# Optimization experiments

Hardware: AMD Instinct MI355X
Metric: run time of the kernel (lower is better)

The kernel has to match this reference:

```python
import jax, jax.numpy as jnp
import numpy as np

B, N, L, D = 256, 128, 2048, 64
ATOM_V, AMINO_V = 2000, 10000
LAYER_GNN, LAYER_CNN, LAYER_OUT = 3, 3, 2
SIDE = 5
WINDOW = 2 * SIDE + 1   # 11 -> conv kernel 23x23, padding 11
N_OUT = 2
EPS = 1e-6


def setup_inputs() -> dict:
    ks = jax.random.split(jax.random.key(0), 16)
    s = 0.05
    return {
        "atoms": jax.random.randint(ks[0], (B, N), 0, ATOM_V),
        "atoms_mask": jnp.ones((B, N), jnp.float32),
        "adjacency": jax.random.uniform(ks[1], (B, N, N), jnp.float32),
        "amino": jax.random.randint(ks[2], (B, L), 0, AMINO_V),
        "amino_mask": jnp.ones((B, L), jnp.float32),
        "emb_fp": jax.random.normal(ks[3], (ATOM_V, D), jnp.float32) * s,
        "emb_word": jax.random.normal(ks[4], (AMINO_V, D), jnp.float32) * s,
        "W_gnn": jax.random.normal(ks[5], (LAYER_GNN, D, D), jnp.float32) * s,
        "b_gnn": jax.random.normal(ks[6], (LAYER_GNN, D), jnp.float32) * s,
        "conv_k": jax.random.normal(ks[7], (LAYER_CNN, 2 * WINDOW + 1, 2 * WINDOW + 1), jnp.float32) * s,
        "conv_b": jax.random.normal(ks[8], (LAYER_CNN,), jnp.float32) * s,
        "W_att": jax.random.normal(ks[9], (D, D), jnp.float32) * s,
        "b_att": jax.random.normal(ks[10], (D,), jnp.float32) * s,
        "W_out": jax.random.normal(ks[11], (LAYER_OUT, 2 * D, 2 * D), jnp.float32) * s,
        "b_out": jax.random.normal(ks[12], (LAYER_OUT, 2 * D), jnp.float32) * s,
        "W_int": jax.random.normal(ks[13], (N_OUT, 2 * D), jnp.float32) * s,
        "b_int": jax.random.normal(ks[14], (N_OUT,), jnp.float32) * s,
    }


def reference(atoms, atoms_mask, adjacency, amino, amino_mask,
              emb_fp, emb_word, W_gnn, b_gnn, conv_k, conv_b,
              W_att, b_att, W_out, b_out, W_int, b_int):
    # ---- compound vector via GNN over dense adjacency ----
    xs = emb_fp[atoms]                                   # [B,N,D]
    for i in range(LAYER_GNN):
        hs = jax.nn.relu(jnp.einsum('bnd,ed->bne', xs, W_gnn[i]) + b_gnn[i])
        xs = xs + jnp.einsum('bnm,bmd->bnd', adjacency, hs)
    am = atoms_mask[..., None]                           # [B,N,1]
    compound = (jnp.sum(xs * am, axis=1) / (jnp.sum(am, axis=1) + EPS))[:, None, :]  # [B,1,D]

    # ---- protein vector via attention-CNN ----
    ps = emb_word[amino][:, None]                        # [B,1,L,D] (NCHW)
    for i in range(LAYER_CNN):
        y = jax.lax.conv_general_dilated(
            ps, conv_k[i][None, None], (1, 1),
            [(WINDOW, WINDOW), (WINDOW, WINDOW)],
            dimension_numbers=('NCHW', 'OIHW', 'NCHW'))
        ps = jax.nn.relu(y + conv_b[i])
    ps = ps[:, 0]                                        # [B,L,D]
    h = jax.nn.relu(jnp.einsum('bqd,ed->bqe', compound, W_att) + b_att)  # [B,1,D]
    hs = jax.nn.relu(jnp.einsum('bld,ed->ble', ps, W_att) + b_att)       # [B,L,D]
    pm = amino_mask[..., None]                           # [B,L,1]
    hs = hs * pm
    weights = jnp.tanh(jnp.einsum('bqd,bld->bql', h, hs))  # [B,1,L]
    ys = jnp.transpose(weights, (0, 2, 1)) * hs             # [B,L,D]
    protein = (jnp.sum(ys, axis=1) / (jnp.sum(pm, axis=1) + EPS))[:, None, :]  # [B,1,D]

    # ---- fuse and predict ----
    cat = jnp.concatenate([compound, protein], axis=2)[:, 0]  # [B,2D]
    for j in range(LAYER_OUT):
        cat = jax.nn.relu(cat @ W_out[j].T + b_out[j])  # dropout is identity in eval
    return cat @ W_int.T + b_int                          # [B,N_OUT]
```

## Files before the change

### kernel.cpp

```cpp
#include <hip/hip_runtime.h>
#include <hip/hip_bf16.h>
#include <cstdint>
#include <cstddef>

#define BB 256
#define NN 128
#define LL 2048
#define DD 64
#define KS 23
#define CPAD 12
#define EPSF 1e-6f
#define ACH 8

typedef __bf16 v8bf __attribute__((ext_vector_type(8)));
typedef float v4f __attribute__((ext_vector_type(4)));

__device__ __forceinline__ float bf2f(uint32_t u) {
  union { uint32_t i; float f; } c; c.i = u << 16; return c.f;
}
__device__ __forceinline__ uint16_t f2bf(float f) {
  union { float f; uint32_t i; } c; c.f = f;
  uint32_t i = c.i;
  return (uint16_t)((i + 0x7fffu + ((i >> 16) & 1u)) >> 16);
}
__device__ __forceinline__ __bf16 f2bf16(float f) {
  union { uint16_t u; __bf16 h; } c; c.u = f2bf(f); return c.h;
}
__device__ __forceinline__ v8bf cvt8(float4 f0, float4 f1) {
  v8bf r;
  r[0] = (__bf16)f0.x; r[1] = (__bf16)f0.y; r[2] = (__bf16)f0.z; r[3] = (__bf16)f0.w;
  r[4] = (__bf16)f1.x; r[5] = (__bf16)f1.y; r[6] = (__bf16)f1.z; r[7] = (__bf16)f1.w;
  return r;
}

#define XSS 68
#define HTS3 136

__global__ __launch_bounds__(256) void gnn_kernel(
    const int* __restrict__ atoms, const float* __restrict__ atoms_mask,
    const float* __restrict__ adj, const float* __restrict__ emb_fp,
    const float* __restrict__ W_gnn, const float* __restrict__ b_gnn,
    const float* __restrict__ W_att, const float* __restrict__ b_att,
    float* __restrict__ compound, float* __restrict__ hvec_g)
{
  __shared__ float xs[NN * XSS];
  __shared__ uint16_t hsT[DD * HTS3];
  __shared__ float mask_s[NN];
  __shared__ float psum[4][64];
  __shared__ float cvec[64];

  const int b = blockIdx.x;
  const int tid = threadIdx.x;
  const int lane = tid & 63;
  const int w = tid >> 6;
  const int m16 = lane & 15;
  const int s = lane >> 4;

  for (int idx = tid; idx < NN * 16; idx += 256) {
    int n = idx >> 4, c4 = idx & 15;
    int a = atoms[b * NN + n];
    float4 v = ((const float4*)(emb_fp + (size_t)a * DD))[c4];
    *(float4*)(xs + n * XSS + c4 * 4) = v;
  }
  if (tid < NN) mask_s[tid] = atoms_mask[b * NN + tid];
  __syncthreads();

  const int row0 = 32 * w;
  for (int layer = 0; layer < 3; ++layer) {
    v8bf Wf[2][4];
    float bias[4];
    const float* Wl = W_gnn + (size_t)layer * DD * DD;
    #pragma unroll
    for (int nt = 0; nt < 4; ++nt) {
      bias[nt] = b_gnn[layer * DD + nt * 16 + m16];
      #pragma unroll
      for (int kc = 0; kc < 2; ++kc) {
        const float* p = Wl + (size_t)(nt * 16 + m16) * DD + kc * 32 + s * 8;
        Wf[kc][nt] = cvt8(((const float4*)p)[0], ((const float4*)p)[1]);
      }
    }
    float4 araw[8][2];
    const float* adjw = adj + ((size_t)b * NN + row0) * NN;
    #pragma unroll
    for (int kc = 0; kc < 4; ++kc)
      #pragma unroll
      for (int mt = 0; mt < 2; ++mt) {
        const float* p = adjw + (size_t)(mt * 16 + m16) * NN + kc * 32 + s * 8;
        araw[kc * 2 + mt][0] = ((const float4*)p)[0];
        araw[kc * 2 + mt][1] = ((const float4*)p)[1];
      }

    v4f acc[2][4];
    #pragma unroll
    for (int mt = 0; mt < 2; ++mt)
      #pragma unroll
      for (int nt = 0; nt < 4; ++nt)
        acc[mt][nt] = (v4f){bias[nt], bias[nt], bias[nt], bias[nt]};
    #pragma unroll
    for (int kc = 0; kc < 2; ++kc) {
      v8bf Axs[2];
      #pragma unroll
      for (int mt = 0; mt < 2; ++mt) {
        const float* p = xs + (size_t)(row0 + mt * 16 + m16) * XSS + kc * 32 + s * 8;
        Axs[mt] = cvt8(((const float4*)p)[0], ((const float4*)p)[1]);
      }
      #pragma unroll
      for (int mt = 0; mt < 2; ++mt)
        #pragma unroll
        for (int nt = 0; nt < 4; ++nt)
          acc[mt][nt] = __builtin_amdgcn_mfma_f32_16x16x32_bf16(
              Axs[mt], Wf[kc][nt], acc[mt][nt], 0, 0, 0);
    }
    __syncthreads();
    #pragma unroll
    for (int mt = 0; mt < 2; ++mt)
      #pragma unroll
      for (int nt = 0; nt < 4; ++nt) {
        int e = nt * 16 + m16;
        int m = row0 + mt * 16 + s * 4;
        union { uint64_t u; __bf16 h[4]; } pk;
        #pragma unroll
        for (int r = 0; r < 4; ++r)
          pk.h[r] = (__bf16)fmaxf(acc[mt][nt][r], 0.f);
        *(uint64_t*)(hsT + (size_t)e * HTS3 + m) = pk.u;
      }
    __syncthreads();

    v4f acc2[2][4];
    #pragma unroll
    for (int mt = 0; mt < 2; ++mt)
      #pragma unroll
      for (int nt = 0; nt < 4; ++nt)
        #pragma unroll
        for (int r = 0; r < 4; ++r)
          acc2[mt][nt][r] = xs[(size_t)(row0 + mt * 16 + s * 4 + r) * XSS + nt * 16 + m16];
    #pragma unroll
    for (int kc = 0; kc < 4; ++kc) {
      v8bf Aa[2];
      #pragma unroll
      for (int mt = 0; mt < 2; ++mt)
        Aa[mt] = cvt8(araw[kc * 2 + mt][0], araw[kc * 2 + mt][1]);
      v8bf Bh[4];
      #pragma unroll
      for (int nt = 0; nt < 4; ++nt)
        Bh[nt] = *(const v8bf*)(hsT + (size_t)(nt * 16 + m16) * HTS3 + kc * 32 + s * 8);
      #pragma unroll
      for (int mt = 0; mt < 2; ++mt)
        #pragma unroll
        for (int nt = 0; nt < 4; ++nt)
          acc2[mt][nt] = __builtin_amdgcn_mfma_f32_16x16x32_bf16(
              Aa[mt], Bh[nt], acc2[mt][nt], 0, 0, 0);
    }
    #pragma unroll
    for (int mt = 0; mt < 2; ++mt)
      #pragma unroll
      for (int nt = 0; nt < 4; ++nt)
        #pragma unroll
        for (int r = 0; r < 4; ++r)
          xs[(size_t)(row0 + mt * 16 + s * 4 + r) * XSS + nt * 16 + m16] = acc2[mt][nt][r];
  }

  float pr = 0.f;
  for (int i = 0; i < 32; ++i) {
    int n = row0 + i;
    pr = fmaf(mask_s[n], xs[(size_t)n * XSS + lane], pr);
  }
  psum[w][lane] = pr;
  __syncthreads();
  if (tid < 64) {
    float ssum = psum[0][tid] + psum[1][tid] + psum[2][tid] + psum[3][tid];
    float den = 0.f;
    #pragma unroll 8
    for (int i = 0; i < NN; ++i) den += mask_s[i];
    float c = ssum / (den + EPSF);
    compound[b * DD + tid] = c;
    cvec[tid] = c;
  }
  __syncthreads();
  if (tid < 64) {
    float a = b_att[tid];
    const float* wr = W_att + (size_t)tid * DD;
    #pragma unroll
    for (int d4 = 0; d4 < 16; ++d4) {
      float4 w4 = ((const float4*)wr)[d4];
      float4 c4 = ((const float4*)cvec)[d4];
      a = fmaf(w4.x, c4.x, a); a = fmaf(w4.y, c4.y, a);
      a = fmaf(w4.z, c4.z, a); a = fmaf(w4.w, c4.w, a);
    }
    hvec_g[b * DD + tid] = fmaxf(a, 0.f);
  }
}

__global__ __launch_bounds__(64) void bfrag_kernel(
    const float* __restrict__ conv_k, uint16_t* __restrict__ btab)
{
  const int layer = blockIdx.x;
  const int lane = threadIdx.x;
  const int s = lane >> 4, n = lane & 15;
  for (int kk = 0; kk < 30; ++kk) {
    int k8 = kk * 4 + s;
    int i = k8 / 5;
    int c8 = k8 - i * 5;
    #pragma unroll
    for (int j = 0; j < 8; ++j) {
      int c = c8 * 8 + j;
      int jj = c - n - 1;
      float v = (i < KS && jj >= 0 && jj < KS)
                    ? conv_k[layer * KS * KS + i * KS + jj] : 0.f;
      btab[(((size_t)layer * 30 + kk) * 64 + lane) * 8 + j] = f2bf(v);
    }
  }
}

#define TW 88
#define TROWS 86

__global__ __launch_bounds__(256, 2) void conv_mfma_kernel(
    const uint16_t* __restrict__ in, uint16_t* __restrict__ out,
    const uint16_t* __restrict__ btab, const float* __restrict__ conv_b,
    const int* __restrict__ amino, const float* __restrict__ emb_word,
    int layer, int gmode)
{
  __shared__ uint16_t tile[TROWS * TW];
  const int tid = threadIdx.x;
  const int l0 = blockIdx.x * 64;
  const int b  = blockIdx.y;
  const int lane = tid & 63;
  const int g = tid >> 6;

  v8bf bfr[30];
  const uint16_t* bt = btab + (size_t)layer * 30 * 512 + lane * 8;
  #pragma unroll
  for (int kk = 0; kk < 30; ++kk)
    bfr[kk] = *(const v8bf*)(bt + kk * 512);

  for (int i = tid; i < TROWS * 6; i += 256) {
    int r = i / 6, h = i - r * 6;
    int off = (h < 3) ? h * 4 : 76 + (h - 3) * 4;
    *(uint2*)(tile + r * TW + off) = make_uint2(0u, 0u);
  }
  const uint16_t* inb = in + (size_t)b * LL * DD;
  for (int idx = tid; idx < TROWS * 8; idx += 256) {
    int t = idx >> 3, c8 = idx & 7;
    int gl = l0 - 11 + t;
    uint16_t* dst = tile + t * TW + CPAD + c8 * 8;
    if (gl >= 0 && gl < LL) {
      if (gmode) {
        int a = amino[b * LL + gl];
        const float* src = emb_word + (size_t)a * DD + c8 * 8;
        float4 f0 = ((const float4*)src)[0];
        float4 f1 = ((const float4*)src)[1];
        union { uint2 u2[2]; uint16_t h[8]; } pk;
        pk.h[0] = f2bf(f0.x); pk.h[1] = f2bf(f0.y);
        pk.h[2] = f2bf(f0.z); pk.h[3] = f2bf(f0.w);
        pk.h[4] = f2bf(f1.x); pk.h[5] = f2bf(f1.y);
        pk.h[6] = f2bf(f1.z); pk.h[7] = f2bf(f1.w);
        *(uint2*)(dst)     = pk.u2[0];
        *(uint2*)(dst + 4) = pk.u2[1];
      } else {
        uint4 v = *(const uint4*)(inb + (size_t)gl * DD + c8 * 8);
        *(uint2*)(dst)     = make_uint2(v.x, v.y);
        *(uint2*)(dst + 4) = make_uint2(v.z, v.w);
      }
    } else {
      *(uint2*)(dst)     = make_uint2(0u, 0u);
      *(uint2*)(dst + 4) = make_uint2(0u, 0u);
    }
  }
  __syncthreads();

  const int s = lane >> 4;
  const int m16 = lane & 15;
  v4f acc[4];
  #pragma unroll
  for (int m = 0; m < 4; ++m) acc[m] = (v4f){0.f, 0.f, 0.f, 0.f};

  #pragma unroll
  for (int kk = 0; kk < 30; ++kk) {
    int k8 = kk * 4 + s;
    int i = k8 / 5;
    int c8 = k8 - i * 5;
    const uint16_t* ap = tile + (m16 + i) * TW + 16 * g + c8 * 8;
    v8bf a0 = *(const v8bf*)(ap);
    v8bf a1 = *(const v8bf*)(ap + 16 * TW);
    v8bf a2 = *(const v8bf*)(ap + 32 * TW);
    v8bf a3 = *(const v8bf*)(ap + 48 * TW);
    acc[0] = __builtin_amdgcn_mfma_f32_16x16x32_bf16(a0, bfr[kk], acc[0], 0, 0, 0);
    acc[1] = __builtin_amdgcn_mfma_f32_16x16x32_bf16(a1, bfr[kk], acc[1], 0, 0, 0);
    acc[2] = __builtin_amdgcn_mfma_f32_16x16x32_bf16(a2, bfr[kk], acc[2], 0, 0, 0);
    acc[3] = __builtin_amdgcn_mfma_f32_16x16x32_bf16(a3, bfr[kk], acc[3], 0, 0, 0);
  }

  const float bias = conv_b[layer];
  uint16_t* outb = out + ((size_t)b * LL + l0) * DD + 16 * g + m16;
  #pragma unroll
  for (int m = 0; m < 4; ++m) {
    #pragma unroll
    for (int r = 0; r < 4; ++r) {
      int row = m * 16 + s * 4 + r;
      outb[(size_t)row * DD] = f2bf(fmaxf(acc[m][r] + bias, 0.f));
    }
  }
}

#define HTS2 66

__global__ __launch_bounds__(256) void attn_part_kernel(
    const uint16_t* __restrict__ ps, const float* __restrict__ amino_mask,
    const float* __restrict__ hvec_g, const float* __restrict__ W_att,
    const float* __restrict__ b_att, float* __restrict__ pacc_part,
    float* __restrict__ msum_part)
{
  __shared__ float ht[4][32 * HTS2];
  __shared__ float pm_s[4][64];
  __shared__ float wv_s[4][32];
  __shared__ float hv_s[64];

  const int chunk = blockIdx.x;
  const int b = blockIdx.y;
  const int tid = threadIdx.x;
  const int lane = tid & 63;
  const int w = tid >> 6;
  const int m16 = lane & 15;
  const int s = lane >> 4;

  v8bf bfrB[2][4];
  float bias[4];
  #pragma unroll
  for (int nt = 0; nt < 4; ++nt) {
    bias[nt] = b_att[nt * 16 + m16];
    const float* wr = W_att + (size_t)(nt * 16 + m16) * DD + s * 8;
    #pragma unroll
    for (int kc = 0; kc < 2; ++kc) {
      float4 f0 = ((const float4*)(wr + kc * 32))[0];
      float4 f1 = ((const float4*)(wr + kc * 32))[1];
      bfrB[kc][nt] = cvt8(f0, f1);
    }
  }
  if (tid < 64) hv_s[tid] = hvec_g[b * DD + tid];

  const int rowbase = chunk * 256 + w * 64;
  const float* pmb = amino_mask + (size_t)b * LL;
  pm_s[w][lane] = pmb[rowbase + lane];
  const float macc = pm_s[w][lane];
  __syncthreads();

  float pacc[4] = {0.f, 0.f, 0.f, 0.f};
  const uint16_t* psb = ps + ((size_t)b * LL + rowbase) * DD;

  #pragma unroll
  for (int step = 0; step < 2; ++step) {
    const uint16_t* pr = psb + (size_t)step * 32 * DD;
    v8bf A[2][2];
    #pragma unroll
    for (int mt = 0; mt < 2; ++mt)
      #pragma unroll
      for (int kc = 0; kc < 2; ++kc)
        A[mt][kc] = *(const v8bf*)(pr + (mt * 16 + m16) * DD + kc * 32 + s * 8);

    v4f acc[2][4];
    #pragma unroll
    for (int mt = 0; mt < 2; ++mt)
      #pragma unroll
      for (int nt = 0; nt < 4; ++nt)
        acc[mt][nt] = (v4f){0.f, 0.f, 0.f, 0.f};
    #pragma unroll
    for (int kc = 0; kc < 2; ++kc)
      #pragma unroll
      for (int mt = 0; mt < 2; ++mt)
        #pragma unroll
        for (int nt = 0; nt < 4; ++nt)
          acc[mt][nt] = __builtin_amdgcn_mfma_f32_16x16x32_bf16(
              A[mt][kc], bfrB[kc][nt], acc[mt][nt], 0, 0, 0);

    float vals[2][4][4];
    float* htw = ht[w];
    #pragma unroll
    for (int mt = 0; mt < 2; ++mt)
      #pragma unroll
      for (int r = 0; r < 4; ++r) {
        int row = mt * 16 + s * 4 + r;
        float pm = pm_s[w][step * 32 + row];
        #pragma unroll
        for (int nt = 0; nt < 4; ++nt) {
          float v = fmaxf(acc[mt][nt][r] + bias[nt], 0.f) * pm;
          vals[mt][nt][r] = v;
          htw[row * HTS2 + nt * 16 + m16] = v;
        }
      }
    __syncthreads();

    {
      int row = lane & 31, eh = lane >> 5;
      const float* hr = ht[w] + row * HTS2 + eh * 32;
      const float* hv = hv_s + eh * 32;
      float d = 0.f;
      #pragma unroll
      for (int t = 0; t < 8; ++t) {
        float4 hh = *(const float4*)(hr + 4 * t);
        float4 vv = *(const float4*)(hv + 4 * t);
        d = fmaf(hh.x, vv.x, d); d = fmaf(hh.y, vv.y, d);
        d = fmaf(hh.z, vv.z, d); d = fmaf(hh.w, vv.w, d);
      }
      d += __shfl_xor(d, 32);
      float wt = tanhf(d);
      if (lane < 32) wv_s[w][row] = wt;
    }
    __syncthreads();

    #pragma unroll
    for (int mt = 0; mt < 2; ++mt)
      #pragma unroll
      for (int r = 0; r < 4; ++r) {
        float wt = wv_s[w][mt * 16 + s * 4 + r];
        #pragma unroll
        for (int nt = 0; nt < 4; ++nt)
          pacc[nt] = fmaf(wt, vals[mt][nt][r], pacc[nt]);
      }
    __syncthreads();
  }

  const size_t idx = ((size_t)b * ACH + chunk) * 4 + w;
  #pragma unroll
  for (int nt = 0; nt < 4; ++nt) {
    float p = pacc[nt];
    p += __shfl_xor(p, 16);
    p += __shfl_xor(p, 32);
    if (m16 == lane)
      pacc_part[idx * 64 + nt * 16 + lane] = p;
  }
  float m = macc;
  #pragma unroll
  for (int off = 1; off < 64; off <<= 1) m += __shfl_xor(m, off);
  if (lane == 0) msum_part[idx] = m;
}

__global__ __launch_bounds__(128) void attn_final_kernel(
    const float* __restrict__ compound, const float* __restrict__ pacc_part,
    const float* __restrict__ msum_part, const float* __restrict__ W_out,
    const float* __restrict__ b_out, const float* __restrict__ W_int,
    const float* __restrict__ b_int, float* __restrict__ outp)
{
  __shared__ float cat[128];
  __shared__ float cat2[128];
  const int b = blockIdx.x;
  const int tid = threadIdx.x;

  if (tid < 64) {
    float p = 0.f, den = 0.f;
    #pragma unroll 4
    for (int c = 0; c < ACH * 4; ++c) {
      p += pacc_part[((size_t)b * ACH * 4 + c) * 64 + tid];
      den += msum_part[b * ACH * 4 + c];
    }
    cat[tid] = compound[b * DD + tid];
    cat[64 + tid] = p / (den + EPSF);
  }
  __syncthreads();
  {
    float a = b_out[tid];
    const float* wr = W_out + (size_t)tid * 128;
    #pragma unroll 8
    for (int dd = 0; dd < 128; ++dd) a = fmaf(wr[dd], cat[dd], a);
    cat2[tid] = fmaxf(a, 0.f);
  }
  __syncthreads();
  {
    float a = b_out[128 + tid];
    const float* wr = W_out + 128 * 128 + (size_t)tid * 128;
    #pragma unroll 8
    for (int dd = 0; dd < 128; ++dd) a = fmaf(wr[dd], cat2[dd], a);
    __syncthreads();
    cat[tid] = fmaxf(a, 0.f);
  }
  __syncthreads();
  if (tid < 2) {
    float a = b_int[tid];
    const float* wr = W_int + (size_t)tid * 128;
    #pragma unroll 8
    for (int dd = 0; dd < 128; ++dd) a = fmaf(wr[dd], cat[dd], a);
    outp[b * 2 + tid] = a;
  }
}

extern "C" void kernel_launch(void* const* d_in, const int* in_sizes, int n_in,
                              void* d_out, int out_size, void* d_ws, size_t ws_size,
                              hipStream_t stream) {
  const int*   atoms      = (const int*)d_in[0];
  const float* atoms_mask = (const float*)d_in[1];
  const float* adjacency  = (const float*)d_in[2];
  const int*   amino      = (const int*)d_in[3];
  const float* amino_mask = (const float*)d_in[4];
  const float* emb_fp     = (const float*)d_in[5];
  const float* emb_word   = (const float*)d_in[6];
  const float* W_gnn      = (const float*)d_in[7];
  const float* b_gnn      = (const float*)d_in[8];
  const float* conv_k     = (const float*)d_in[9];
  const float* conv_b     = (const float*)d_in[10];
  const float* W_att      = (const float*)d_in[11];
  const float* b_att      = (const float*)d_in[12];
  const float* W_out      = (const float*)d_in[13];
  const float* b_out      = (const float*)d_in[14];
  const float* W_int      = (const float*)d_in[15];
  const float* b_int      = (const float*)d_in[16];
  float* out = (float*)d_out;

  char* ws = (char*)d_ws;
  const size_t ps_bytes = (size_t)BB * LL * DD * 2;
  float*    compound  = (float*)ws;
  uint16_t* ps_a      = (uint16_t*)(ws + 65536);
  uint16_t* ps_b      = (uint16_t*)(ws + 65536 + ps_bytes);
  uint16_t* btab      = (uint16_t*)(ws + 65536 + 2 * ps_bytes);
  float*    hvec_g    = (float*)(ws + 65536 + 2 * ps_bytes + 131072);
  float*    pacc_part = (float*)ps_a;
  float*    msum_part = (float*)((char*)ps_a + (size_t)BB * ACH * 4 * 64 * 4);

  bfrag_kernel<<<3, 64, 0, stream>>>(conv_k, btab);
  gnn_kernel<<<BB, 256, 0, stream>>>(atoms, atoms_mask, adjacency, emb_fp,
                                     W_gnn, b_gnn, W_att, b_att,
                                     compound, hvec_g);
  conv_mfma_kernel<<<dim3(LL / 64, BB), 256, 0, stream>>>(ps_a, ps_b, btab, conv_b,
                                                          amino, emb_word, 0, 1);
  conv_mfma_kernel<<<dim3(LL / 64, BB), 256, 0, stream>>>(ps_b, ps_a, btab, conv_b,
                                                          amino, emb_word, 1, 0);
  conv_mfma_kernel<<<dim3(LL / 64, BB), 256, 0, stream>>>(ps_a, ps_b, btab, conv_b,
                                                          amino, emb_word, 2, 0);
  attn_part_kernel<<<dim3(ACH, BB), 256, 0, stream>>>(ps_b, amino_mask, hvec_g,
                                                      W_att, b_att,
                                                      pacc_part, msum_part);
  attn_final_kernel<<<BB, 128, 0, stream>>>(compound, pacc_part, msum_part,
                                            W_out, b_out, W_int, b_int, out);
}
```

Before: 421.8 us.

## Fuse GNN into first conv launch and fuse last conv with attention

The GNN work now runs as an extra column of blocks inside the first conv launch, so it overlaps with the convolution instead of running as its own kernel. The third conv layer is fused with the attention-partial computation: the conv output tile is written to shared memory as bf16 and fed straight into the W_att MFMA, tanh weighting and partial sums. This removes a full write and re-read of the last activation tensor plus two launches. In exchange the conv kernel's shared memory grows to about 54KB to fit the GNN path, which may lower occupancy, and attn_final must now reduce 128 partials per batch instead of 32.

```diff
diff --git a/kernel.cpp b/kernel.cpp
--- a/kernel.cpp
+++ b/kernel.cpp
@@ -10,7 +10,6 @@
 #define KS 23
 #define CPAD 12
 #define EPSF 1e-6f
-#define ACH 8
 
 typedef __bf16 v8bf __attribute__((ext_vector_type(8)));
 typedef float v4f __attribute__((ext_vector_type(4)));
@@ -22,9 +21,6 @@
   union { float f; uint32_t i; } c; c.f = f;
   uint32_t i = c.i;
   return (uint16_t)((i + 0x7fffu + ((i >> 16) & 1u)) >> 16);
-}
-__device__ __forceinline__ __bf16 f2bf16(float f) {
-  union { uint16_t u; __bf16 h; } c; c.u = f2bf(f); return c.h;
 }
 __device__ __forceinline__ v8bf cvt8(float4 f0, float4 f1) {
   v8bf r;
@@ -36,20 +32,20 @@
 #define XSS 68
 #define HTS3 136
 
-__global__ __launch_bounds__(256) void gnn_kernel(
+__device__ void gnn_body(char* smem,
     const int* __restrict__ atoms, const float* __restrict__ atoms_mask,
     const float* __restrict__ adj, const float* __restrict__ emb_fp,
     const float* __restrict__ W_gnn, const float* __restrict__ b_gnn,
     const float* __restrict__ W_att, const float* __restrict__ b_att,
     float* __restrict__ compound, float* __restrict__ hvec_g)
 {
-  __shared__ float xs[NN * XSS];
-  __shared__ uint16_t hsT[DD * HTS3];
-  __shared__ float mask_s[NN];
-  __shared__ float psum[4][64];
-  __shared__ float cvec[64];
-
-  const int b = blockIdx.x;
+  float*    xs     = (float*)smem;
+  uint16_t* hsT    = (uint16_t*)(smem + 34816);
+  float*    mask_s = (float*)(smem + 52224);
+  float*    psum   = (float*)(smem + 52736);
+  float*    cvec   = (float*)(smem + 53760);
+
+  const int b = blockIdx.y;
   const int tid = threadIdx.x;
   const int lane = tid & 63;
   const int w = tid >> 6;
@@ -165,10 +161,11 @@
     int n = row0 + i;
     pr = fmaf(mask_s[n], xs[(size_t)n * XSS + lane], pr);
   }
-  psum[w][lane] = pr;
+  psum[w * 64 + lane] = pr;
   __syncthreads();
   if (tid < 64) {
-    float ssum = psum[0][tid] + psum[1][tid] + psum[2][tid] + psum[3][tid];
+    float ssum = psum[0 * 64 + tid] + psum[1 * 64 + tid]
+               + psum[2 * 64 + tid] + psum[3 * 64 + tid];
     float den = 0.f;
     #pragma unroll 8
     for (int i = 0; i < NN; ++i) den += mask_s[i];
@@ -215,15 +212,27 @@
 #define TW 88
 #define TROWS 86
 
-__global__ __launch_bounds__(256, 2) void conv_mfma_kernel(
+__global__ __launch_bounds__(256, 2) void conv01_kernel(
     const uint16_t* __restrict__ in, uint16_t* __restrict__ out,
     const uint16_t* __restrict__ btab, const float* __restrict__ conv_b,
     const int* __restrict__ amino, const float* __restrict__ emb_word,
+    const int* __restrict__ atoms, const float* __restrict__ atoms_mask,
+    const float* __restrict__ adj, const float* __restrict__ emb_fp,
+    const float* __restrict__ W_gnn, const float* __restrict__ b_gnn,
+    const float* __restrict__ W_att, const float* __restrict__ b_att,
+    float* __restrict__ compound, float* __restrict__ hvec_g,
     int layer, int gmode)
 {
-  __shared__ uint16_t tile[TROWS * TW];
+  __shared__ __align__(16) char smem[54016];
+  if (gmode && blockIdx.x == 0) {
+    gnn_body(smem, atoms, atoms_mask, adj, emb_fp, W_gnn, b_gnn,
+             W_att, b_att, compound, hvec_g);
+    return;
+  }
+  uint16_t* tile = (uint16_t*)smem;
+  const int tl = gmode ? (int)blockIdx.x - 1 : (int)blockIdx.x;
   const int tid = threadIdx.x;
-  const int l0 = blockIdx.x * 64;
+  const int l0 = tl * 64;
   const int b  = blockIdx.y;
   const int lane = tid & 63;
   const int g = tid >> 6;
@@ -303,136 +312,172 @@
   }
 }
 
-#define HTS2 66
-
-__global__ __launch_bounds__(256) void attn_part_kernel(
-    const uint16_t* __restrict__ ps, const float* __restrict__ amino_mask,
+#define T2S 68
+
+__global__ __launch_bounds__(256, 2) void conv2attn_kernel(
+    const uint16_t* __restrict__ in, const uint16_t* __restrict__ btab,
+    const float* __restrict__ conv_b, const float* __restrict__ amino_mask,
     const float* __restrict__ hvec_g, const float* __restrict__ W_att,
-    const float* __restrict__ b_att, float* __restrict__ pacc_part,
-    float* __restrict__ msum_part)
+    const float* __restrict__ b_att, float* __restrict__ pacc_g,
+    float* __restrict__ msum_g)
 {
-  __shared__ float ht[4][32 * HTS2];
-  __shared__ float pm_s[4][64];
-  __shared__ float wv_s[4][32];
-  __shared__ float hv_s[64];
-
-  const int chunk = blockIdx.x;
-  const int b = blockIdx.y;
+  __shared__ __align__(16) char smem[33312];
+  uint16_t* tile  = (uint16_t*)smem;
+  float*    ht    = (float*)(smem + 15136);
+  float*    wv_s  = (float*)(smem + 32544);
+  float*    pm_s  = (float*)(smem + 32800);
+  float*    hv_s  = (float*)(smem + 33056);
+
+  const int layer = 2;
   const int tid = threadIdx.x;
+  const int tl = blockIdx.x;
+  const int l0 = tl * 64;
+  const int b  = blockIdx.y;
   const int lane = tid & 63;
-  const int w = tid >> 6;
+  const int g = tid >> 6;
+
+  v8bf bfr[30];
+  const uint16_t* bt = btab + (size_t)layer * 30 * 512 + lane * 8;
+  #pragma unroll
+  for (int kk = 0; kk < 30; ++kk)
+    bfr[kk] = *(const v8bf*)(bt + kk * 512);
+
+  for (int i = tid; i < TROWS * 6; i += 256) {
+    int r = i / 6, h = i - r * 6;
+    int off = (h < 3) ? h * 4 : 76 + (h - 3) * 4;
+    *(uint2*)(tile + r * TW + off) = make_uint2(0u, 0u);
+  }
+  const uint16_t* inb = in + (size_t)b * LL * DD;
+  for (int idx = tid; idx < TROWS * 8; idx += 256) {
+    int t = idx >> 3, c8 = idx & 7;
+    int gl = l0 - 11 + t;
+    uint16_t* dst = tile + t * TW + CPAD + c8 * 8;
+    if (gl >= 0 && gl < LL) {
+      uint4 v = *(const uint4*)(inb + (size_t)gl * DD + c8 * 8);
+      *(uint2*)(dst)     = make_uint2(v.x, v.y);
+      *(uint2*)(dst + 4) = make_uint2(v.z, v.w);
+    } else {
+      *(uint2*)(dst)     = make_uint2(0u, 0u);
+      *(uint2*)(dst + 4) = make_uint2(0u, 0u);
+    }
+  }
+  if (tid < 64) {
+    pm_s[tid] = amino_mask[(size_t)b * LL + l0 + tid];
+    hv_s[tid] = hvec_g[b * DD + tid];
+  }
+  __syncthreads();
+
+  const int s = lane >> 4;
   const int m16 = lane & 15;
-  const int s = lane >> 4;
-
-  v8bf bfrB[2][4];
-  float bias[4];
+  v4f acc[4];
+  #pragma unroll
+  for (int m = 0; m < 4; ++m) acc[m] = (v4f){0.f, 0.f, 0.f, 0.f};
+
+  #pragma unroll
+  for (int kk = 0; kk < 30; ++kk) {
+    int k8 = kk * 4 + s;
+    int i = k8 / 5;
+    int c8 = k8 - i * 5;
+    const uint16_t* ap = tile + (m16 + i) * TW + 16 * g + c8 * 8;
+    v8bf a0 = *(const v8bf*)(ap);
+    v8bf a1 = *(const v8bf*)(ap + 16 * TW);
+    v8bf a2 = *(const v8bf*)(ap + 32 * TW);
+    v8bf a3 = *(const v8bf*)(ap + 48 * TW);
+    acc[0] = __builtin_amdgcn_mfma_f32_16x16x32_bf16(a0, bfr[kk], acc[0], 0, 0, 0);
+    acc[1] = __builtin_amdgcn_mfma_f32_16x16x32_bf16(a1, bfr[kk], acc[1], 0, 0, 0);
+    acc[2] = __builtin_amdgcn_mfma_f32_16x16x32_bf16(a2, bfr[kk], acc[2], 0, 0, 0);
+    acc[3] = __builtin_amdgcn_mfma_f32_16x16x32_bf16(a3, bfr[kk], acc[3], 0, 0, 0);
+  }
+
+  const float cbias = conv_b[layer];
+  __syncthreads();
+  uint16_t* tile2 = tile;
+  #pragma unroll
+  for (int m = 0; m < 4; ++m)
+    #pragma unroll
+    for (int r = 0; r < 4; ++r) {
+      int row = m * 16 + s * 4 + r;
+      tile2[row * T2S + (row & 1) * 4 + 16 * g + m16] =
+          f2bf(fmaxf(acc[m][r] + cbias, 0.f));
+    }
+  v8bf Wf[2][4];
+  float batt[4];
   #pragma unroll
   for (int nt = 0; nt < 4; ++nt) {
-    bias[nt] = b_att[nt * 16 + m16];
+    batt[nt] = b_att[nt * 16 + m16];
     const float* wr = W_att + (size_t)(nt * 16 + m16) * DD + s * 8;
     #pragma unroll
     for (int kc = 0; kc < 2; ++kc) {
       float4 f0 = ((const float4*)(wr + kc * 32))[0];
       float4 f1 = ((const float4*)(wr + kc * 32))[1];
-      bfrB[kc][nt] = cvt8(f0, f1);
-    }
-  }
-  if (tid < 64) hv_s[tid] = hvec_g[b * DD + tid];
-
-  const int rowbase = chunk * 256 + w * 64;
-  const float* pmb = amino_mask + (size_t)b * LL;
-  pm_s[w][lane] = pmb[rowbase + lane];
-  const float macc = pm_s[w][lane];
-  __syncthreads();
-
+      Wf[kc][nt] = cvt8(f0, f1);
+    }
+  }
+  __syncthreads();
+
+  v4f aac[4];
+  #pragma unroll
+  for (int nt = 0; nt < 4; ++nt) aac[nt] = (v4f){0.f, 0.f, 0.f, 0.f};
+  #pragma unroll
+  for (int kc = 0; kc < 2; ++kc) {
+    int arow = 16 * g + m16;
+    const uint16_t* ap = tile2 + arow * T2S + (arow & 1) * 4 + kc * 32 + s * 8;
+    union { uint2 u2[2]; v8bf v; } A;
+    A.u2[0] = *(const uint2*)(ap);
+    A.u2[1] = *(const uint2*)(ap + 4);
+    #pragma unroll
+    for (int nt = 0; nt < 4; ++nt)
+      aac[nt] = __builtin_amdgcn_mfma_f32_16x16x32_bf16(A.v, Wf[kc][nt], aac[nt], 0, 0, 0);
+  }
+  float vals[4][4];
+  float* htw = ht + g * (16 * 68);
+  #pragma unroll
+  for (int r = 0; r < 4; ++r) {
+    int rl = s * 4 + r;
+    float pm = pm_s[16 * g + rl];
+    #pragma unroll
+    for (int nt = 0; nt < 4; ++nt) {
+      float v = fmaxf(aac[nt][r] + batt[nt], 0.f) * pm;
+      vals[nt][r] = v;
+      htw[rl * 68 + nt * 16 + m16] = v;
+    }
+  }
+  {
+    int row = lane >> 2, eq = lane & 3;
+    const float* hr = htw + row * 68 + eq * 16;
+    const float* hv = hv_s + eq * 16;
+    float d = 0.f;
+    #pragma unroll
+    for (int t = 0; t < 4; ++t) {
+      float4 hh = *(const float4*)(hr + 4 * t);
+      float4 vv = *(const float4*)(hv + 4 * t);
+      d = fmaf(hh.x, vv.x, d); d = fmaf(hh.y, vv.y, d);
+      d = fmaf(hh.z, vv.z, d); d = fmaf(hh.w, vv.w, d);
+    }
+    d += __shfl_xor(d, 1);
+    d += __shfl_xor(d, 2);
+    if (eq == 0) wv_s[g * 16 + row] = tanhf(d);
+  }
   float pacc[4] = {0.f, 0.f, 0.f, 0.f};
-  const uint16_t* psb = ps + ((size_t)b * LL + rowbase) * DD;
-
-  #pragma unroll
-  for (int step = 0; step < 2; ++step) {
-    const uint16_t* pr = psb + (size_t)step * 32 * DD;
-    v8bf A[2][2];
-    #pragma unroll
-    for (int mt = 0; mt < 2; ++mt)
-      #pragma unroll
-      for (int kc = 0; kc < 2; ++kc)
-        A[mt][kc] = *(const v8bf*)(pr + (mt * 16 + m16) * DD + kc * 32 + s * 8);
-
-    v4f acc[2][4];
-    #pragma unroll
-    for (int mt = 0; mt < 2; ++mt)
-      #pragma unroll
-      for (int nt = 0; nt < 4; ++nt)
-        acc[mt][nt] = (v4f){0.f, 0.f, 0.f, 0.f};
-    #pragma unroll
-    for (int kc = 0; kc < 2; ++kc)
-      #pragma unroll
-      for (int mt = 0; mt < 2; ++mt)
-        #pragma unroll
-        for (int nt = 0; nt < 4; ++nt)
-          acc[mt][nt] = __builtin_amdgcn_mfma_f32_16x16x32_bf16(
-              A[mt][kc], bfrB[kc][nt], acc[mt][nt], 0, 0, 0);
-
-    float vals[2][4][4];
-    float* htw = ht[w];
-    #pragma unroll
-    for (int mt = 0; mt < 2; ++mt)
-      #pragma unroll
-      for (int r = 0; r < 4; ++r) {
-        int row = mt * 16 + s * 4 + r;
-        float pm = pm_s[w][step * 32 + row];
-        #pragma unroll
-        for (int nt = 0; nt < 4; ++nt) {
-          float v = fmaxf(acc[mt][nt][r] + bias[nt], 0.f) * pm;
-          vals[mt][nt][r] = v;
-          htw[row * HTS2 + nt * 16 + m16] = v;
-        }
-      }
-    __syncthreads();
-
-    {
-      int row = lane & 31, eh = lane >> 5;
-      const float* hr = ht[w] + row * HTS2 + eh * 32;
-      const float* hv = hv_s + eh * 32;
-      float d = 0.f;
-      #pragma unroll
-      for (int t = 0; t < 8; ++t) {
-        float4 hh = *(const float4*)(hr + 4 * t);
-        float4 vv = *(const float4*)(hv + 4 * t);
-        d = fmaf(hh.x, vv.x, d); d = fmaf(hh.y, vv.y, d);
-        d = fmaf(hh.z, vv.z, d); d = fmaf(hh.w, vv.w, d);
-      }
-      d += __shfl_xor(d, 32);
-      float wt = tanhf(d);
-      if (lane < 32) wv_s[w][row] = wt;
-    }
-    __syncthreads();
-
-    #pragma unroll
-    for (int mt = 0; mt < 2; ++mt)
-      #pragma unroll
-      for (int r = 0; r < 4; ++r) {
-        float wt = wv_s[w][mt * 16 + s * 4 + r];
-        #pragma unroll
-        for (int nt = 0; nt < 4; ++nt)
-          pacc[nt] = fmaf(wt, vals[mt][nt][r], pacc[nt]);
-      }
-    __syncthreads();
-  }
-
-  const size_t idx = ((size_t)b * ACH + chunk) * 4 + w;
+  #pragma unroll
+  for (int r = 0; r < 4; ++r) {
+    float wt = wv_s[g * 16 + s * 4 + r];
+    #pragma unroll
+    for (int nt = 0; nt < 4; ++nt)
+      pacc[nt] = fmaf(wt, vals[nt][r], pacc[nt]);
+  }
+  const size_t sl = (size_t)(b * 32 + tl) * 4 + g;
   #pragma unroll
   for (int nt = 0; nt < 4; ++nt) {
     float p = pacc[nt];
     p += __shfl_xor(p, 16);
     p += __shfl_xor(p, 32);
-    if (m16 == lane)
-      pacc_part[idx * 64 + nt * 16 + lane] = p;
-  }
-  float m = macc;
-  #pragma unroll
-  for (int off = 1; off < 64; off <<= 1) m += __shfl_xor(m, off);
-  if (lane == 0) msum_part[idx] = m;
+    if (lane < 16) pacc_g[sl * 64 + nt * 16 + lane] = p;
+  }
+  float mm = (lane < 16) ? pm_s[16 * g + lane] : 0.f;
+  mm += __shfl_xor(mm, 1); mm += __shfl_xor(mm, 2);
+  mm += __shfl_xor(mm, 4); mm += __shfl_xor(mm, 8);
+  if (lane == 0) msum_g[sl] = mm;
 }
 
 __global__ __launch_bounds__(128) void attn_final_kernel(
@@ -448,10 +493,10 @@
 
   if (tid < 64) {
     float p = 0.f, den = 0.f;
-    #pragma unroll 4
-    for (int c = 0; c < ACH * 4; ++c) {
-      p += pacc_part[((size_t)b * ACH * 4 + c) * 64 + tid];
-      den += msum_part[b * ACH * 4 + c];
+    #pragma unroll 8
+    for (int c = 0; c < 128; ++c) {
+      p += pacc_part[((size_t)b * 128 + c) * 64 + tid];
+      den += msum_part[b * 128 + c];
     }
     cat[tid] = compound[b * DD + tid];
     cat[64 + tid] = p / (den + EPSF);
@@ -512,22 +557,20 @@
   uint16_t* ps_b      = (uint16_t*)(ws + 65536 + ps_bytes);
   uint16_t* btab      = (uint16_t*)(ws + 65536 + 2 * ps_bytes);
   float*    hvec_g    = (float*)(ws + 65536 + 2 * ps_bytes + 131072);
-  float*    pacc_part = (float*)ps_a;
-  float*    msum_part = (float*)((char*)ps_a + (size_t)BB * ACH * 4 * 64 * 4);
+  float*    pacc_g = (float*)ps_b;
+  float*    msum_g = (float*)((char*)ps_b + (size_t)BB * 32 * 4 * 64 * 4);
 
   bfrag_kernel<<<3, 64, 0, stream>>>(conv_k, btab);
-  gnn_kernel<<<BB, 256, 0, stream>>>(atoms, atoms_mask, adjacency, emb_fp,
-                                     W_gnn, b_gnn, W_att, b_att,
-                                     compound, hvec_g);
-  conv_mfma_kernel<<<dim3(LL / 64, BB), 256, 0, stream>>>(ps_a, ps_b, btab, conv_b,
-                                                          amino, emb_word, 0, 1);
-  conv_mfma_kernel<<<dim3(LL / 64, BB), 256, 0, stream>>>(ps_b, ps_a, btab, conv_b,
-                                                          amino, emb_word, 1, 0);
-  conv_mfma_kernel<<<dim3(LL / 64, BB), 256, 0, stream>>>(ps_a, ps_b, btab, conv_b,
-                                                          amino, emb_word, 2, 0);
-  attn_part_kernel<<<dim3(ACH, BB), 256, 0, stream>>>(ps_b, amino_mask, hvec_g,
-                                                      W_att, b_att,
-                                                      pacc_part, msum_part);
-  attn_final_kernel<<<BB, 128, 0, stream>>>(compound, pacc_part, msum_part,
+  conv01_kernel<<<dim3(33, BB), 256, 0, stream>>>(
+      ps_a, ps_b, btab, conv_b, amino, emb_word,
+      atoms, atoms_mask, adjacency, emb_fp, W_gnn, b_gnn, W_att, b_att,
+      compound, hvec_g, 0, 1);
+  conv01_kernel<<<dim3(32, BB), 256, 0, stream>>>(
+      ps_b, ps_a, btab, conv_b, amino, emb_word,
+      atoms, atoms_mask, adjacency, emb_fp, W_gnn, b_gnn, W_att, b_att,
+      compound, hvec_g, 1, 0);
+  conv2attn_kernel<<<dim3(32, BB), 256, 0, stream>>>(
+      ps_a, btab, conv_b, amino_mask, hvec_g, W_att, b_att, pacc_g, msum_g);
+  attn_final_kernel<<<BB, 128, 0, stream>>>(compound, pacc_g, msum_g,
                                             W_out, b_out, W_int, b_int, out);
 }
```

Measured after the change: 487.2 us. 15.5% more time.

## Stage conv output through LDS for coalesced stores, fold bfrag into gnn kernel

Applied to the files above, without the earlier changes.

The conv epilogue now writes results into the shared tile and then stores 16-byte vectors per row, instead of scattered 2-byte stores strided by 64 elements. This is meant to cut the cost of uncoalesced global writes. The B-fragment table build moves into the first three blocks of the gnn kernel, removing one kernel launch. Conv occupancy is raised to 3 blocks per SIMD via launch bounds, which may force register spills given the 30 preloaded fragments.

```diff
diff --git a/kernel.cpp b/kernel.cpp
--- a/kernel.cpp
+++ b/kernel.cpp
@@ -23,9 +23,6 @@
   uint32_t i = c.i;
   return (uint16_t)((i + 0x7fffu + ((i >> 16) & 1u)) >> 16);
 }
-__device__ __forceinline__ __bf16 f2bf16(float f) {
-  union { uint16_t u; __bf16 h; } c; c.u = f2bf(f); return c.h;
-}
 __device__ __forceinline__ v8bf cvt8(float4 f0, float4 f1) {
   v8bf r;
   r[0] = (__bf16)f0.x; r[1] = (__bf16)f0.y; r[2] = (__bf16)f0.z; r[3] = (__bf16)f0.w;
@@ -41,6 +38,7 @@
     const float* __restrict__ adj, const float* __restrict__ emb_fp,
     const float* __restrict__ W_gnn, const float* __restrict__ b_gnn,
     const float* __restrict__ W_att, const float* __restrict__ b_att,
+    const float* __restrict__ conv_k, uint16_t* __restrict__ btab,
     float* __restrict__ compound, float* __restrict__ hvec_g)
 {
   __shared__ float xs[NN * XSS];
@@ -189,33 +187,29 @@
     }
     hvec_g[b * DD + tid] = fmaxf(a, 0.f);
   }
-}
-
-__global__ __launch_bounds__(64) void bfrag_kernel(
-    const float* __restrict__ conv_k, uint16_t* __restrict__ btab)
-{
-  const int layer = blockIdx.x;
-  const int lane = threadIdx.x;
-  const int s = lane >> 4, n = lane & 15;
-  for (int kk = 0; kk < 30; ++kk) {
-    int k8 = kk * 4 + s;
-    int i = k8 / 5;
-    int c8 = k8 - i * 5;
-    #pragma unroll
-    for (int j = 0; j < 8; ++j) {
-      int c = c8 * 8 + j;
-      int jj = c - n - 1;
-      float v = (i < KS && jj >= 0 && jj < KS)
-                    ? conv_k[layer * KS * KS + i * KS + jj] : 0.f;
-      btab[(((size_t)layer * 30 + kk) * 64 + lane) * 8 + j] = f2bf(v);
+
+  if (b < 3) {
+    for (int kk = w; kk < 30; kk += 4) {
+      int k8 = kk * 4 + s;
+      int i = k8 / 5;
+      int c8k = k8 - i * 5;
+      #pragma unroll
+      for (int j = 0; j < 8; ++j) {
+        int c = c8k * 8 + j;
+        int jj = c - m16 - 1;
+        float v = (i < KS && jj >= 0 && jj < KS)
+                      ? conv_k[b * KS * KS + i * KS + jj] : 0.f;
+        btab[(((size_t)b * 30 + kk) * 64 + lane) * 8 + j] = f2bf(v);
+      }
     }
   }
 }
 
 #define TW 88
 #define TROWS 86
-
-__global__ __launch_bounds__(256, 2) void conv_mfma_kernel(
+#define OTS 72
+
+__global__ __launch_bounds__(256, 3) void conv_kernel(
     const uint16_t* __restrict__ in, uint16_t* __restrict__ out,
     const uint16_t* __restrict__ btab, const float* __restrict__ conv_b,
     const int* __restrict__ amino, const float* __restrict__ emb_word,
@@ -292,14 +286,21 @@
   }
 
   const float bias = conv_b[layer];
-  uint16_t* outb = out + ((size_t)b * LL + l0) * DD + 16 * g + m16;
-  #pragma unroll
-  for (int m = 0; m < 4; ++m) {
+  __syncthreads();
+  uint16_t* ot = tile;
+  #pragma unroll
+  for (int m = 0; m < 4; ++m)
     #pragma unroll
     for (int r = 0; r < 4; ++r) {
       int row = m * 16 + s * 4 + r;
-      outb[(size_t)row * DD] = f2bf(fmaxf(acc[m][r] + bias, 0.f));
-    }
+      ot[row * OTS + 16 * g + m16] = f2bf(fmaxf(acc[m][r] + bias, 0.f));
+    }
+  __syncthreads();
+  uint16_t* outb = out + ((size_t)b * LL + l0) * DD;
+  for (int i = tid; i < 512; i += 256) {
+    int row = i >> 3, c8 = i & 7;
+    uint4 v = *(const uint4*)(ot + row * OTS + c8 * 8);
+    *(uint4*)(outb + (size_t)row * DD + c8 * 8) = v;
   }
 }
 
@@ -515,16 +516,15 @@
   float*    pacc_part = (float*)ps_a;
   float*    msum_part = (float*)((char*)ps_a + (size_t)BB * ACH * 4 * 64 * 4);
 
-  bfrag_kernel<<<3, 64, 0, stream>>>(conv_k, btab);
   gnn_kernel<<<BB, 256, 0, stream>>>(atoms, atoms_mask, adjacency, emb_fp,
                                      W_gnn, b_gnn, W_att, b_att,
-                                     compound, hvec_g);
-  conv_mfma_kernel<<<dim3(LL / 64, BB), 256, 0, stream>>>(ps_a, ps_b, btab, conv_b,
-                                                          amino, emb_word, 0, 1);
-  conv_mfma_kernel<<<dim3(LL / 64, BB), 256, 0, stream>>>(ps_b, ps_a, btab, conv_b,
-                                                          amino, emb_word, 1, 0);
-  conv_mfma_kernel<<<dim3(LL / 64, BB), 256, 0, stream>>>(ps_a, ps_b, btab, conv_b,
-                                                          amino, emb_word, 2, 0);
+                                     conv_k, btab, compound, hvec_g);
+  conv_kernel<<<dim3(32, BB), 256, 0, stream>>>(ps_a, ps_b, btab, conv_b,
+                                                amino, emb_word, 0, 1);
+  conv_kernel<<<dim3(32, BB), 256, 0, stream>>>(ps_b, ps_a, btab, conv_b,
+                                                amino, emb_word, 1, 0);
+  conv_kernel<<<dim3(32, BB), 256, 0, stream>>>(ps_a, ps_b, btab, conv_b,
+                                                amino, emb_word, 2, 0);
   attn_part_kernel<<<dim3(ACH, BB), 256, 0, stream>>>(ps_b, amino_mask, hvec_g,
                                                       W_att, b_att,
                                                       pacc_part, msum_part);
```

After: 405.5 us. -3.9%, faster.
